# Kernel tuning notes

Measured on AMD Instinct MI355X. Metric: run time of the kernel, lower is better.

## Reference

```python
import jax, jax.numpy as jnp
import numpy as np

R = 16      # grid resolution per axis (G = R**3 voxels)
K = 8       # num KNN neighbors per voxel
H = 64      # num_hidden
NB = 2      # num conv blocks
EPS = 1e-5


def _conv3d(x, w, b):
    # x: [B,C,D,H,W], w: [O,I,3,3,3]
    y = jax.lax.conv_general_dilated(
        x, w, window_strides=(1, 1, 1), padding='SAME',
        dimension_numbers=('NCDHW', 'OIDHW', 'NCDHW'))
    return y + b[None, :, None, None, None]


def _bn(x):
    # training-mode BatchNorm3d statistics (no affine), per channel
    m = x.mean(axis=(0, 2, 3, 4), keepdims=True)
    v = x.var(axis=(0, 2, 3, 4), keepdims=True)
    return (x - m) * jax.lax.rsqrt(v + EPS)


def _forward(pos, x, pe_w1, pe_b1, pe_w2, pe_b2, f_w, f_b, up_w, up_b,
             conv_w, conv_b, on_g, on_b, ro_w, ro_b):
    B, N, _ = pos.shape
    # ---- Gridifier: coordinate grid over domain [-1, 1]^3 ----
    g1 = jnp.linspace(-1.0, 1.0, R, dtype=pos.dtype)
    grid = jnp.stack(jnp.meshgrid(g1, g1, g1, indexing='ij'), axis=-1).reshape(-1, 3)  # [G,3]
    # ---- brute-force KNN: points -> grid voxels (per graph) ----
    gn = jnp.sum(grid * grid, axis=-1)          # [G]
    pn = jnp.sum(pos * pos, axis=-1)            # [B,N]
    d = gn[None, :, None] + pn[:, None, :] - 2.0 * jnp.einsum('gc,bnc->bgn', grid, pos)  # [B,G,N]
    idx = jax.lax.top_k(jax.lax.stop_gradient(-d), K)[1]  # [B,G,K] nearest point indices
    b_ix = jnp.arange(B)[:, None, None]
    p_nb = pos[b_ix, idx]                       # [B,G,K,3] neighbor positions
    f_nb = x[b_ix, idx]                         # [B,G,K,Cin] neighbor features
    # ---- BipartiteConv: position-conditioned messages, mean aggregation ----
    rel = p_nb - grid[None, :, None, :]         # relative positions [B,G,K,3]
    pe = jax.nn.gelu(rel @ pe_w1 + pe_b1) @ pe_w2 + pe_b2   # position embed [B,G,K,H]
    msg = pe * (f_nb @ f_w + f_b)               # multiplicative conditioning [B,G,K,H]
    agg = msg.mean(axis=2)                      # [B,G,H]
    h = jax.nn.gelu(agg @ up_w + up_b)          # update net [B,G,H]
    # reshape(B,R,R,R,H).permute(0,4,3,2,1) -> NCDHW
    vol = h.reshape(B, R, R, R, H).transpose(0, 4, 3, 2, 1)  # [B,H,R,R,R]
    # ---- ConvNet3D: residual blocks, maxpool after block 0 ----
    for i in range(NB):
        h1 = jax.nn.relu(_bn(_conv3d(vol, conv_w[i, 0], conv_b[i, 0])))
        h2 = _bn(_conv3d(h1, conv_w[i, 1], conv_b[i, 1]))
        vol = jax.nn.relu(vol + h2)
        if i == 0:
            vol = jax.lax.reduce_window(vol, -jnp.inf, jax.lax.max,
                                        (1, 1, 2, 2, 2), (1, 1, 2, 2, 2), 'VALID')
    out = _bn(vol) * on_g[None, :, None, None, None] + on_b[None, :, None, None, None]
    # ---- mean readout pool + linear head ----
    pooled = out.mean(axis=(2, 3, 4))           # [B,H]
    return pooled @ ro_w + ro_b                 # [B,out_channels]


def setup_inputs() -> dict:
    key = jax.random.key(0)
    ks = jax.random.split(key, 10)
    B, N, Cin, OUT = 4, 4096, 3, 16
    s = 0.05
    return {
        'pos': jax.random.uniform(ks[0], (B, N, 3), jnp.float32, -1.0, 1.0),
        'x': jax.random.normal(ks[1], (B, N, Cin), jnp.float32),
        'pe_w1': jax.random.normal(ks[2], (3, H), jnp.float32) * 0.3,
        'pe_b1': jnp.zeros((H,), jnp.float32),
        'pe_w2': jax.random.normal(ks[3], (H, H), jnp.float32) * s,
        'pe_b2': jnp.zeros((H,), jnp.float32),
        'f_w': jax.random.normal(ks[4], (Cin, H), jnp.float32) * 0.3,
        'f_b': jnp.zeros((H,), jnp.float32),
        'up_w': jax.random.normal(ks[5], (H, H), jnp.float32) * s,
        'up_b': jnp.zeros((H,), jnp.float32),
        'conv_w': jax.random.normal(ks[6], (NB, 2, H, H, 3, 3, 3), jnp.float32) * s,
        'conv_b': jnp.zeros((NB, 2, H), jnp.float32),
        'on_g': jnp.ones((H,), jnp.float32),
        'on_b': jnp.zeros((H,), jnp.float32),
        'ro_w': jax.random.normal(ks[7], (H, OUT), jnp.float32) * s,
        'ro_b': jnp.zeros((OUT,), jnp.float32),
    }


def reference(pos, x, pe_w1, pe_b1, pe_w2, pe_b2, f_w, f_b, up_w, up_b,
              conv_w, conv_b, on_g, on_b, ro_w, ro_b):
    return _forward(pos, x, pe_w1, pe_b1, pe_w2, pe_b2, f_w, f_b, up_w, up_b,
                    conv_w, conv_b, on_g, on_b, ro_w, ro_b)
```

## Files before the change

kernel.cpp:

```cpp
#include <hip/hip_runtime.h>

#define ULL unsigned long long
typedef unsigned short ush;
typedef __attribute__((ext_vector_type(8))) short s8v;
typedef __attribute__((ext_vector_type(4))) float f4v;

#define BB 4
#define NP 4096
#define HH 64
#define EPSF 1e-5f

#define WH_OFF      0u
#define WL_OFF      221184u
#define WT_PER_CONV 110592u
#define IDX_OFF     442368u
#define VOL0_OFF    573440u
#define V0H_OFF     2066432u
#define V0L_OFF     2812928u
#define T1_OFF      3559424u
#define VOL1_OFF    4608000u
#define V1H_OFF     4864000u
#define V1L_OFF     4992000u
#define T3_OFF      5120000u
#define STATS_OFF   5251072u
#define CELLS_OFF   5251968u
#define SPOS_OFF    5268368u
#define MW_OFF      5333904u

#define ZN_V0   373248u
#define ZN_V1   64000u
#define ZN_ST   224u
#define ZN_ALL  (ZN_V0 + ZN_V1 + ZN_ST)

__device__ __forceinline__ ush f2bf(float f) {
  unsigned u = __float_as_uint(f);
  return (ush)((u + 0x7FFFu + ((u >> 16) & 1u)) >> 16);
}
__device__ __forceinline__ float bf2f(ush h) { return __uint_as_float(((unsigned)h) << 16); }

__device__ __forceinline__ float gelu_tanh(float v) {
  float inner = 0.7978845608028654f * (v + 0.044715f * v * v * v);
  return 0.5f * v * (1.0f + tanhf(inner));
}

__device__ __forceinline__ float lin16(int i) {
  return -1.0f + (float)i * (2.0f / 15.0f);
}

__global__ __launch_bounds__(256) void k_prep(const float* __restrict__ cw,
                                              const float* __restrict__ pw2,
                                              const float* __restrict__ upw,
                                              ush* __restrict__ wh,
                                              ush* __restrict__ wl,
                                              ush* __restrict__ mw,
                                              float* __restrict__ ws) {
  unsigned i = blockIdx.x * 256u + threadIdx.x;
  float4 z = make_float4(0.f, 0.f, 0.f, 0.f);
  if (i < ZN_V0) ((float4*)(ws + V0H_OFF))[i] = z;
  else if (i < ZN_V0 + ZN_V1) ((float4*)(ws + V1H_OFF))[i - ZN_V0] = z;
  else if (i < ZN_ALL) ((float4*)(ws + STATS_OFF))[i - ZN_V0 - ZN_V1] = z;
  if (i < 442368u) {
    unsigned conv = i / WT_PER_CONV;
    unsigned r = i - conv * WT_PER_CONV;
    unsigned off = r >> 12;
    unsigned q = r & 4095u;
    unsigned co = q >> 6, ci = q & 63u;
    float w = cw[(conv * 4096u + co * 64u + ci) * 27u + off];
    ush hi = f2bf(w);
    wh[i] = hi;
    wl[i] = f2bf(w - bf2f(hi));
  } else if (i < 450560u) {
    unsigned t = i - 442368u;
    unsigned mat = t >> 12, r = t & 4095u;
    unsigned co = r >> 6, ci = r & 63u;
    const float* src = mat ? upw : pw2;
    float w = src[ci * 64u + co];
    ush hi = f2bf(w);
    mw[mat * 8192u + co * 64u + ci] = hi;
    mw[mat * 8192u + 4096u + co * 64u + ci] = f2bf(w - bf2f(hi));
  }
}

__global__ __launch_bounds__(256) void k_bin(const float* __restrict__ pos,
                                             int* __restrict__ cellStart,
                                             float4* __restrict__ sortedPos) {
  __shared__ int cnt[4096];
  __shared__ int wsum[4];
  int tid = threadIdx.x;
  int b = blockIdx.x;
  const float* pb = pos + b * NP * 3;
  for (int i = tid; i < 4096; i += 256) cnt[i] = 0;
  __syncthreads();
#pragma unroll
  for (int t = 0; t < 16; ++t) {
    int p = t * 256 + tid;
    float px = pb[3 * p], py = pb[3 * p + 1], pz = pb[3 * p + 2];
    int c0 = (int)floorf((px + 1.0f) * 7.5f + 0.5f);
    int c1 = (int)floorf((py + 1.0f) * 7.5f + 0.5f);
    int c2 = (int)floorf((pz + 1.0f) * 7.5f + 0.5f);
    c0 = min(max(c0, 0), 15); c1 = min(max(c1, 0), 15); c2 = min(max(c2, 0), 15);
    atomicAdd(&cnt[(c0 * 16 + c1) * 16 + c2], 1);
  }
  __syncthreads();
  int base = tid * 16;
  int loc[16];
  int run = 0;
#pragma unroll
  for (int j = 0; j < 16; ++j) { loc[j] = run; run += cnt[base + j]; }
  int lane = tid & 63, wv = tid >> 6;
  int inc = run;
  for (int d = 1; d < 64; d <<= 1) {
    int o = __shfl_up(inc, d, 64);
    if (lane >= d) inc += o;
  }
  if (lane == 63) wsum[wv] = inc;
  __syncthreads();
  int woff = 0;
  for (int w = 0; w < wv; ++w) woff += wsum[w];
  int excl = woff + inc - run;
  __syncthreads();
  int stv[16];
#pragma unroll
  for (int j = 0; j < 16; ++j) {
    stv[j] = excl + loc[j];
    cellStart[b * 4097 + base + j] = stv[j];
  }
#pragma unroll
  for (int j = 0; j < 16; ++j) cnt[base + j] = stv[j];
  if (tid == 0) cellStart[b * 4097 + 4096] = NP;
  __syncthreads();
#pragma unroll
  for (int t = 0; t < 16; ++t) {
    int p = t * 256 + tid;
    float px = pb[3 * p], py = pb[3 * p + 1], pz = pb[3 * p + 2];
    int c0 = (int)floorf((px + 1.0f) * 7.5f + 0.5f);
    int c1 = (int)floorf((py + 1.0f) * 7.5f + 0.5f);
    int c2 = (int)floorf((pz + 1.0f) * 7.5f + 0.5f);
    c0 = min(max(c0, 0), 15); c1 = min(max(c1, 0), 15); c2 = min(max(c2, 0), 15);
    int slot = atomicAdd(&cnt[(c0 * 16 + c1) * 16 + c2], 1);
    sortedPos[b * 4096 + slot] = make_float4(px, py, pz, __int_as_float(p));
  }
}

__device__ __forceinline__ void ins8(ULL* kk, ULL key) {
  if (key < kk[7]) {
    kk[7] = key;
#pragma unroll
    for (int q = 7; q >= 1; --q) {
      ULL a = kk[q - 1], c = kk[q];
      bool sw = c < a;
      kk[q - 1] = sw ? c : a;
      kk[q] = sw ? a : c;
    }
  }
}
__device__ __forceinline__ ULL merge8(ULL* kk, int sub) {
  ULL win = 0;
#pragma unroll
  for (int r = 0; r < 8; ++r) {
    ULL m = kk[0];
#pragma unroll
    for (int s = 1; s < 8; s <<= 1) {
      ULL o = __shfl_xor(m, s, 64);
      m = (o < m) ? o : m;
    }
    if (kk[0] == m) {
#pragma unroll
      for (int q = 0; q < 7; ++q) kk[q] = kk[q + 1];
      kk[7] = ~0ULL;
    }
    if (sub == r) win = m;
  }
  return win;
}

__device__ __forceinline__ void scan_cell(const int* __restrict__ cs,
                                          const float4* __restrict__ sp,
                                          int cell, float gx, float gy, float gz,
                                          float gn, ULL* kk) {
  int st = cs[cell], en = cs[cell + 1];
  for (int p = st; p < en; ++p) {
    float4 c = sp[p];
    float pn = c.x * c.x + c.y * c.y + c.z * c.z;
    float dt = gx * c.x + gy * c.y + gz * c.z;
    float d = (gn + pn) - 2.0f * dt;
    unsigned u = __float_as_uint(d);
    u ^= (unsigned)((int)u >> 31) | 0x80000000u;
    ins8(kk, ((ULL)u << 32) | (unsigned)__float_as_uint(c.w));
  }
}

__global__ __launch_bounds__(256) void k_knn3(const int* __restrict__ cellStart,
                                              const float4* __restrict__ sortedPos,
                                              int* __restrict__ idxo) {
  int tid = threadIdx.x;
  int sub = tid & 7;
  int vox = blockIdx.x * 32 + (tid >> 3);
  int b = vox >> 12;
  int g = vox & 4095;
  int ii = g >> 8, jj = (g >> 4) & 15, kkc = g & 15;
  float gx = lin16(ii), gy = lin16(jj), gz = lin16(kkc);
  float gn = gx * gx + gy * gy + gz * gz;
  const int* cs = cellStart + b * 4097;
  const float4* sp = sortedPos + b * 4096;
  ULL kk[8];
#pragma unroll
  for (int q = 0; q < 8; ++q) kk[q] = ~0ULL;
  for (int t = sub; t < 125; t += 8) {
    int dz = t / 25, r25 = t - dz * 25;
    int a = ii + dz - 2, c1 = jj + (r25 / 5) - 2, c2 = kkc + (r25 % 5) - 2;
    if (((unsigned)a > 15u) | ((unsigned)c1 > 15u) | ((unsigned)c2 > 15u)) continue;
    scan_cell(cs, sp, (a * 16 + c1) * 16 + c2, gx, gy, gz, gn, kk);
  }
  ULL win = merge8(kk, sub);
  float bnd2 = 2.5f * (2.0f / 15.0f) - 1e-5f;
  unsigned ub2 = __float_as_uint(bnd2 * bnd2) | 0x80000000u;
  ULL w7 = __shfl(win, 7, 8);
  if (w7 >= ((ULL)ub2 << 32)) {
#pragma unroll
    for (int q = 0; q < 8; ++q) kk[q] = ~0ULL;
    for (int t = sub; t < 1331; t += 8) {
      int dz = t / 121, r = t - dz * 121;
      int a = ii + dz - 5, c1 = jj + (r / 11) - 5, c2 = kkc + (r % 11) - 5;
      if (((unsigned)a > 15u) | ((unsigned)c1 > 15u) | ((unsigned)c2 > 15u)) continue;
      scan_cell(cs, sp, (a * 16 + c1) * 16 + c2, gx, gy, gz, gn, kk);
    }
    win = merge8(kk, sub);
    float bnd5 = 5.5f * (2.0f / 15.0f) - 1e-5f;
    unsigned ub5 = __float_as_uint(bnd5 * bnd5) | 0x80000000u;
    w7 = __shfl(win, 7, 8);
    if (w7 >= ((ULL)ub5 << 32)) {
#pragma unroll
      for (int q = 0; q < 8; ++q) kk[q] = ~0ULL;
      for (int p = sub; p < NP; p += 8) {
        float4 c = sp[p];
        float pn = c.x * c.x + c.y * c.y + c.z * c.z;
        float dt = gx * c.x + gy * c.y + gz * c.z;
        float d = (gn + pn) - 2.0f * dt;
        unsigned u = __float_as_uint(d);
        u ^= (unsigned)((int)u >> 31) | 0x80000000u;
        ins8(kk, ((ULL)u << 32) | (unsigned)__float_as_uint(c.w));
      }
      win = merge8(kk, sub);
    }
  }
  idxo[(((b << 12) | g) << 3) + sub] = (int)(win & 0xFFFFFFFFULL);
}

__global__ __launch_bounds__(256) void k_mlp2(
    const float* __restrict__ pos, const float* __restrict__ xf,
    const float* __restrict__ w1, const float* __restrict__ b1,
    const float* __restrict__ b2v, const float* __restrict__ fw,
    const float* __restrict__ fb, const float* __restrict__ ub,
    const ush* __restrict__ w2tH, const ush* __restrict__ w2tL,
    const ush* __restrict__ uwtH, const ush* __restrict__ uwtL,
    const int* __restrict__ idx, float* __restrict__ vol0,
    ush* __restrict__ v0h, ush* __restrict__ v0l) {
  __shared__ __align__(16) ush lhH[128 * 72];
  __shared__ __align__(16) ush lhL[128 * 72];
  __shared__ __align__(16) float lfe[128 * 68];
  __shared__ __align__(16) ush agH[16 * 72];
  __shared__ __align__(16) ush agL[16 * 72];
  int tid = threadIdx.x, lane = tid & 63, wv = tid >> 6;
  int lm = lane & 15, quad = lane >> 4;
  int b = blockIdx.x >> 8;
  int g0 = (blockIdx.x & 255) << 4;
  s8v BH[8], BL[8], UH[2], UL[2];
#pragma unroll
  for (int n = 0; n < 4; ++n)
#pragma unroll
    for (int ks = 0; ks < 2; ++ks) {
      int o = ((n * 16 + lm) << 6) + ks * 32 + (quad << 3);
      BH[n * 2 + ks] = *(const s8v*)(w2tH + o);
      BL[n * 2 + ks] = *(const s8v*)(w2tL + o);
    }
#pragma unroll
  for (int ks = 0; ks < 2; ++ks) {
    int o = ((wv * 16 + lm) << 6) + ks * 32 + (quad << 3);
    UH[ks] = *(const s8v*)(uwtH + o);
    UL[ks] = *(const s8v*)(uwtL + o);
  }
  float w10 = w1[lane], w11 = w1[64 + lane], w12 = w1[128 + lane], b1c = b1[lane];
  float fw0 = fw[lane], fw1 = fw[64 + lane], fw2 = fw[128 + lane], fbc = fb[lane];
  float ubc = ub[wv * 16 + lm];
  float gx = lin16(g0 >> 8), gy = lin16((g0 >> 4) & 15);
  for (int i = 0; i < 32; ++i) {
    int pair = wv * 32 + i;
    int vi = pair >> 3, kk = pair & 7;
    int g = g0 + vi;
    float gz = lin16(vi);
    int p = idx[(((b << 12) | g) << 3) + kk];
    const float* pp = pos + (b * NP + p) * 3;
    float r0 = pp[0] - gx, r1 = pp[1] - gy, r2 = pp[2] - gz;
    float h1 = gelu_tanh(fmaf(r2, w12, fmaf(r1, w11, fmaf(r0, w10, b1c))));
    const float* xp = xf + (b * NP + p) * 3;
    float fe = fmaf(xp[2], fw2, fmaf(xp[1], fw1, fmaf(xp[0], fw0, fbc)));
    ush hi = f2bf(h1);
    lhH[pair * 72 + lane] = hi;
    lhL[pair * 72 + lane] = f2bf(h1 - bf2f(hi));
    lfe[pair * 68 + lane] = fe;
  }
  f4v acc[2][4];
#pragma unroll
  for (int m = 0; m < 2; ++m)
#pragma unroll
    for (int n = 0; n < 4; ++n) acc[m][n] = (f4v){0.f, 0.f, 0.f, 0.f};
#pragma unroll
  for (int m = 0; m < 2; ++m)
#pragma unroll
    for (int ks = 0; ks < 2; ++ks) {
      int ao = (wv * 32 + m * 16 + lm) * 72 + ks * 32 + quad * 8;
      s8v Ah = *(const s8v*)&lhH[ao];
      s8v Al = *(const s8v*)&lhL[ao];
#pragma unroll
      for (int n = 0; n < 4; ++n) {
        acc[m][n] = __builtin_amdgcn_mfma_f32_16x16x32_bf16(Ah, BH[n * 2 + ks], acc[m][n], 0, 0, 0);
        acc[m][n] = __builtin_amdgcn_mfma_f32_16x16x32_bf16(Ah, BL[n * 2 + ks], acc[m][n], 0, 0, 0);
        acc[m][n] = __builtin_amdgcn_mfma_f32_16x16x32_bf16(Al, BH[n * 2 + ks], acc[m][n], 0, 0, 0);
      }
    }
  float b2c[4];
#pragma unroll
  for (int n = 0; n < 4; ++n) b2c[n] = b2v[n * 16 + lm];
#pragma unroll
  for (int m = 0; m < 2; ++m) {
    int vox = wv * 4 + m * 2 + (quad >> 1);
#pragma unroll
    for (int n = 0; n < 4; ++n) {
      float s = 0.0f;
#pragma unroll
      for (int r = 0; r < 4; ++r) {
        int pair = wv * 32 + m * 16 + quad * 4 + r;
        s += (acc[m][n][r] + b2c[n]) * lfe[pair * 68 + n * 16 + lm];
      }
      s += __shfl_xor(s, 16, 64);
      s *= 0.125f;
      if ((quad & 1) == 0) {
        ush hi = f2bf(s);
        agH[vox * 72 + n * 16 + lm] = hi;
        agL[vox * 72 + n * 16 + lm] = f2bf(s - bf2f(hi));
      }
    }
  }
  __syncthreads();
  f4v a2 = (f4v){0.f, 0.f, 0.f, 0.f};
#pragma unroll
  for (int ks = 0; ks < 2; ++ks) {
    int ao = lm * 72 + ks * 32 + quad * 8;
    s8v Ah = *(const s8v*)&agH[ao];
    s8v Al = *(const s8v*)&agL[ao];
    a2 = __builtin_amdgcn_mfma_f32_16x16x32_bf16(Ah, UH[ks], a2, 0, 0, 0);
    a2 = __builtin_amdgcn_mfma_f32_16x16x32_bf16(Ah, UL[ks], a2, 0, 0, 0);
    a2 = __builtin_amdgcn_mfma_f32_16x16x32_bf16(Al, UH[ks], a2, 0, 0, 0);
  }
  int xc = g0 >> 8, yc = (g0 >> 4) & 15;
#pragma unroll
  for (int r = 0; r < 4; ++r) {
    int vox = quad * 4 + r;
    float h = gelu_tanh(a2[r] + ubc);
    int pidx = (((b * 18 + vox + 1) * 18 + yc + 1) * 18 + xc + 1) * 64 + wv * 16 + lm;
    vol0[pidx] = h;
    ush hi = f2bf(h);
    v0h[pidx] = hi;
    v0l[pidx] = f2bf(h - bf2f(hi));
  }
}

template <int Z>
__global__ __launch_bounds__(256) void k_convm(const ush* __restrict__ vh,
                                               const ush* __restrict__ vl,
                                               const ush* __restrict__ wh,
                                               const ush* __restrict__ wl,
                                               float* __restrict__ out,
                                               float* __restrict__ stats) {
  constexpr int P = Z + 2;
  constexpr int Py = (Z == 16) ? 6 : 10;
  constexpr int Px = (Z == 16) ? 18 : 10;
  constexpr int NV = 3 * Py * Px;
  constexpr int VS = 272;
  __shared__ unsigned char slab[NV * VS];
  __shared__ float ls[64], ls2[64];
  int tid = threadIdx.x;
  int lane = tid & 63, wv = tid >> 6;
  int vbase = blockIdx.x * 64;
  int b = (Z == 16) ? (vbase >> 12) : (vbase >> 9);
  int rem = vbase & (Z * Z * Z - 1);
  int z0 = rem / (Z * Z);
  int y0 = (Z == 16) ? ((rem & 255) >> 4) : 0;
  if (tid < 64) { ls[tid] = 0.0f; ls2[tid] = 0.0f; }
  {
    constexpr int NCH = NV * 8;
    for (int i = tid; i < NCH; i += 256) {
      int v = i >> 3, c = i & 7;
      int lz = v / (Py * Px);
      int r = v - lz * (Py * Px);
      int ly = r / Px, lx = r - ly * Px;
      int g = (((b * P + z0 + lz) * P + (y0 + ly)) * P + lx) * 64 + c * 8;
      *(uint4*)(slab + v * VS + c * 16)       = *(const uint4*)(vh + g);
      *(uint4*)(slab + v * VS + 128 + c * 16) = *(const uint4*)(vl + g);
    }
  }
  __syncthreads();
  int lm = lane & 15, quad = lane >> 4;
  int co = (wv << 4) | lm;
  f4v acc[4];
#pragma unroll
  for (int m = 0; m < 4; ++m) acc[m] = (f4v){0.f, 0.f, 0.f, 0.f};
  for (int off = 0; off < 27; ++off) {
    int dz = off / 9, r9 = off - dz * 9, dy = r9 / 3, dx = r9 - dy * 3;
    const ush* bph = wh + ((off * 64 + co) << 6) + (quad << 3);
    const ush* bpl = wl + ((off * 64 + co) << 6) + (quad << 3);
#pragma unroll
    for (int ks = 0; ks < 2; ++ks) {
      s8v bhf = *(const s8v*)(bph + ks * 32);
      s8v blf = *(const s8v*)(bpl + ks * 32);
#pragma unroll
      for (int m = 0; m < 4; ++m) {
        int lyp, lxp;
        if (Z == 16) { lyp = m + dy; lxp = lm + dx; }
        else         { lyp = 2 * m + (lm >> 3) + dy; lxp = (lm & 7) + dx; }
        int sv = (dz * Py + lyp) * Px + lxp;
        const unsigned char* ap = slab + sv * VS + (quad << 4) + (ks << 6);
        s8v ahf = *(const s8v*)(ap);
        s8v alf = *(const s8v*)(ap + 128);
        acc[m] = __builtin_amdgcn_mfma_f32_16x16x32_bf16(ahf, bhf, acc[m], 0, 0, 0);
        acc[m] = __builtin_amdgcn_mfma_f32_16x16x32_bf16(ahf, blf, acc[m], 0, 0, 0);
        acc[m] = __builtin_amdgcn_mfma_f32_16x16x32_bf16(alf, bhf, acc[m], 0, 0, 0);
      }
    }
  }
  float s = 0.0f, s2 = 0.0f;
#pragma unroll
  for (int m = 0; m < 4; ++m) {
    int vx = vbase + (m << 4) + (quad << 2);
#pragma unroll
    for (int r = 0; r < 4; ++r) {
      float v = acc[m][r];
      out[(vx + r) * 64 + co] = v;
      s += v;
      s2 = fmaf(v, v, s2);
    }
  }
  atomicAdd(&ls[co], s);
  atomicAdd(&ls2[co], s2);
  __syncthreads();
  if (tid < 64) {
    atomicAdd(&stats[tid * 2], ls[tid]);
    atomicAdd(&stats[tid * 2 + 1], ls2[tid]);
  }
}

template <int Z>
__global__ __launch_bounds__(256) void k_bnrelu(const float* __restrict__ t,
                                                const float* __restrict__ stats,
                                                ush* __restrict__ outh,
                                                ush* __restrict__ outl,
                                                float inv_cnt) {
  constexpr int P = Z + 2;
  unsigned i = blockIdx.x * 256u + threadIdx.x;
  int c = i & 63;
  int vox = i >> 6;
  int x = vox % Z;
  int q = vox / Z;
  int y = q % Z;
  q /= Z;
  int z = q % Z;
  int b = q / Z;
  float m = stats[c * 2] * inv_cnt;
  float var = stats[c * 2 + 1] * inv_cnt - m * m;
  float rs = 1.0f / sqrtf(var + EPSF);
  float v = (t[i] - m) * rs;
  v = v > 0.0f ? v : 0.0f;
  int pidx = (((b * P + z + 1) * P + y + 1) * P + x + 1) * 64 + c;
  ush hi = f2bf(v);
  outh[pidx] = hi;
  outl[pidx] = f2bf(v - bf2f(hi));
}

__global__ __launch_bounds__(256) void k_residpool(const float* __restrict__ vol0,
                                                   const float* __restrict__ t2,
                                                   const float* __restrict__ stats,
                                                   float* __restrict__ vol1,
                                                   ush* __restrict__ v1h,
                                                   ush* __restrict__ v1l) {
  unsigned i = blockIdx.x * 256u + threadIdx.x;
  int c = i & 63;
  int pv = i >> 6;
  int xp = pv & 7, yp = (pv >> 3) & 7, zp = (pv >> 6) & 7, b = pv >> 9;
  float m = stats[c * 2] * (1.0f / 16384.0f);
  float var = stats[c * 2 + 1] * (1.0f / 16384.0f) - m * m;
  float rs = 1.0f / sqrtf(var + EPSF);
  float best = 0.0f;
  for (int dz = 0; dz < 2; ++dz)
    for (int dy = 0; dy < 2; ++dy)
      for (int dx = 0; dx < 2; ++dx) {
        int z = 2 * zp + dz, y = 2 * yp + dy, x = 2 * xp + dx;
        float a = vol0[(((b * 18 + z + 1) * 18 + y + 1) * 18 + x + 1) * 64 + c];
        float t = t2[(b * 4096 + z * 256 + y * 16 + x) * 64 + c];
        float u = a + (t - m) * rs;
        u = u > 0.0f ? u : 0.0f;
        best = u > best ? u : best;
      }
  int pidx = (((b * 10 + zp + 1) * 10 + yp + 1) * 10 + xp + 1) * 64 + c;
  vol1[pidx] = best;
  ush hi = f2bf(best);
  v1h[pidx] = hi;
  v1l[pidx] = f2bf(best - bf2f(hi));
}

__global__ __launch_bounds__(256) void k_resid2(const float* __restrict__ vol1,
                                                const float* __restrict__ t4,
                                                const float* __restrict__ stats,
                                                float* __restrict__ sF,
                                                float* __restrict__ sB) {
  __shared__ float ls[64], ls2[64];
  if (threadIdx.x < 64) { ls[threadIdx.x] = 0.0f; ls2[threadIdx.x] = 0.0f; }
  __syncthreads();
  unsigned i = blockIdx.x * 256u + threadIdx.x;
  int c = i & 63;
  int pv = i >> 6;
  int x = pv & 7, y = (pv >> 3) & 7, z = (pv >> 6) & 7, b = pv >> 9;
  float m = stats[c * 2] * (1.0f / 2048.0f);
  float var = stats[c * 2 + 1] * (1.0f / 2048.0f) - m * m;
  float rs = 1.0f / sqrtf(var + EPSF);
  float a = vol1[(((b * 10 + z + 1) * 10 + y + 1) * 10 + x + 1) * 64 + c];
  float u = a + (t4[i] - m) * rs;
  u = u > 0.0f ? u : 0.0f;
  atomicAdd(&ls[c], u);
  atomicAdd(&ls2[c], u * u);
  __syncthreads();
  if (threadIdx.x < 64) {
    int cc = threadIdx.x;
    atomicAdd(&sF[cc * 2], ls[cc]);
    atomicAdd(&sF[cc * 2 + 1], ls2[cc]);
    atomicAdd(&sB[b * 64 + cc], ls[cc]);
  }
}

__global__ __launch_bounds__(64) void k_final(const float* __restrict__ sF,
                                              const float* __restrict__ sB,
                                              const float* __restrict__ ong,
                                              const float* __restrict__ onb,
                                              const float* __restrict__ row,
                                              const float* __restrict__ rob,
                                              float* __restrict__ outp) {
  __shared__ float pl[4][64];
  int c = threadIdx.x;
  float m = sF[c * 2] * (1.0f / 2048.0f);
  float var = sF[c * 2 + 1] * (1.0f / 2048.0f) - m * m;
  float rs = 1.0f / sqrtf(var + EPSF);
  float gg = ong[c], bb = onb[c];
  for (int b = 0; b < 4; ++b)
    pl[b][c] = (sB[b * 64 + c] * (1.0f / 512.0f) - m) * rs * gg + bb;
  __syncthreads();
  int b = threadIdx.x >> 4, o = threadIdx.x & 15;
  float s = rob[o];
  for (int j = 0; j < 64; ++j) s = fmaf(pl[b][j], row[j * 16 + o], s);
  outp[b * 16 + o] = s;
}

extern "C" void kernel_launch(void* const* d_in, const int* in_sizes, int n_in,
                              void* d_out, int out_size, void* d_ws, size_t ws_size,
                              hipStream_t stream) {
  (void)in_sizes; (void)n_in; (void)out_size; (void)ws_size;
  const float* pos = (const float*)d_in[0];
  const float* xf  = (const float*)d_in[1];
  const float* pw1 = (const float*)d_in[2];
  const float* pb1 = (const float*)d_in[3];
  const float* pw2 = (const float*)d_in[4];
  const float* pb2 = (const float*)d_in[5];
  const float* fw  = (const float*)d_in[6];
  const float* fb  = (const float*)d_in[7];
  const float* uw  = (const float*)d_in[8];
  const float* ubp = (const float*)d_in[9];
  const float* cw  = (const float*)d_in[10];
  const float* ong = (const float*)d_in[12];
  const float* onb = (const float*)d_in[13];
  const float* row = (const float*)d_in[14];
  const float* rob = (const float*)d_in[15];

  float* ws   = (float*)d_ws;
  ush*   wh   = (ush*)(ws + WH_OFF);
  ush*   wl   = (ush*)(ws + WL_OFF);
  int*   idx  = (int*)(ws + IDX_OFF);
  float* vol0 = ws + VOL0_OFF;
  ush*   v0h  = (ush*)(ws + V0H_OFF);
  ush*   v0l  = (ush*)(ws + V0L_OFF);
  float* t1   = ws + T1_OFF;
  float* vol1 = ws + VOL1_OFF;
  ush*   v1h  = (ush*)(ws + V1H_OFF);
  ush*   v1l  = (ush*)(ws + V1L_OFF);
  float* t3   = ws + T3_OFF;
  float* sA   = ws + STATS_OFF;
  float* sF   = sA + 512;
  float* sB   = sF + 128;
  int*   cellStart = (int*)(ws + CELLS_OFF);
  float4* sortedPos = (float4*)(ws + SPOS_OFF);
  ush*   mw   = (ush*)(ws + MW_OFF);

  k_prep<<<1760, 256, 0, stream>>>(cw, pw2, uw, wh, wl, mw, ws);
  k_bin<<<4, 256, 0, stream>>>(pos, cellStart, sortedPos);
  k_knn3<<<512, 256, 0, stream>>>(cellStart, sortedPos, idx);
  k_mlp2<<<1024, 256, 0, stream>>>(pos, xf, pw1, pb1, pb2, fw, fb, ubp,
                                   mw, mw + 4096, mw + 8192, mw + 12288,
                                   idx, vol0, v0h, v0l);
  k_convm<16><<<256, 256, 0, stream>>>(v0h, v0l, wh, wl, t1, sA);
  k_bnrelu<16><<<4096, 256, 0, stream>>>(t1, sA, v0h, v0l, 1.0f / 16384.0f);
  k_convm<16><<<256, 256, 0, stream>>>(v0h, v0l, wh + WT_PER_CONV, wl + WT_PER_CONV,
                                       t1, sA + 128);
  k_residpool<<<512, 256, 0, stream>>>(vol0, t1, sA + 128, vol1, v1h, v1l);
  k_convm<8><<<32, 256, 0, stream>>>(v1h, v1l, wh + 2 * WT_PER_CONV,
                                     wl + 2 * WT_PER_CONV, t3, sA + 256);
  k_bnrelu<8><<<512, 256, 0, stream>>>(t3, sA + 256, v1h, v1l, 1.0f / 2048.0f);
  k_convm<8><<<32, 256, 0, stream>>>(v1h, v1l, wh + 3 * WT_PER_CONV,
                                     wl + 3 * WT_PER_CONV, t3, sA + 384);
  k_resid2<<<512, 256, 0, stream>>>(vol1, t3, sA + 384, sF, sB);
  k_final<<<1, 64, 0, stream>>>(sF, sB, ong, onb, row, rob, (float*)d_out);
}
```

Measured before the change: 367.2 us.

## Tile KNN over 4x4x4 voxel blocks with shared candidate buffer

KNN now assigns each block a 4x4x4 voxel tile. The block stages every point from the surrounding cell region in shared memory, and each voxel is scanned by 4 lanes instead of 8. The fallback bound is computed from the staged region's distance to its edges. The weight prep kernel now reads conv weights coalesced and scatters the writes, and the MLP kernel gathers neighbor pos/features once into shared memory. These changes aim to cut redundant global loads, at the cost of more per-thread insertion work and some shared-memory pressure.

```diff
diff --git a/kernel.cpp b/kernel.cpp
--- a/kernel.cpp
+++ b/kernel.cpp
@@ -62,13 +62,15 @@
   if (i < 442368u) {
     unsigned conv = i / WT_PER_CONV;
     unsigned r = i - conv * WT_PER_CONV;
-    unsigned off = r >> 12;
-    unsigned q = r & 4095u;
-    unsigned co = q >> 6, ci = q & 63u;
-    float w = cw[(conv * 4096u + co * 64u + ci) * 27u + off];
+    unsigned co = r / 1728u;
+    unsigned r2 = r - co * 1728u;
+    unsigned ci = r2 / 27u;
+    unsigned off = r2 - ci * 27u;
+    float w = cw[i];
     ush hi = f2bf(w);
-    wh[i] = hi;
-    wl[i] = f2bf(w - bf2f(hi));
+    unsigned dst = conv * WT_PER_CONV + (off * 64u + co) * 64u + ci;
+    wh[dst] = hi;
+    wl[dst] = f2bf(w - bf2f(hi));
   } else if (i < 450560u) {
     unsigned t = i - 442368u;
     unsigned mat = t >> 12, r = t & 4095u;
@@ -154,24 +156,19 @@
     }
   }
 }
-__device__ __forceinline__ ULL merge8(ULL* kk, int sub) {
-  ULL win = 0;
+__device__ __forceinline__ void merge4(ULL* kk, int sub, ULL& win0, ULL& win1) {
 #pragma unroll
   for (int r = 0; r < 8; ++r) {
     ULL m = kk[0];
-#pragma unroll
-    for (int s = 1; s < 8; s <<= 1) {
-      ULL o = __shfl_xor(m, s, 64);
-      m = (o < m) ? o : m;
-    }
+    ULL o = __shfl_xor(m, 1, 64); m = (o < m) ? o : m;
+    o = __shfl_xor(m, 2, 64);     m = (o < m) ? o : m;
     if (kk[0] == m) {
 #pragma unroll
       for (int q = 0; q < 7; ++q) kk[q] = kk[q + 1];
       kk[7] = ~0ULL;
     }
-    if (sub == r) win = m;
-  }
-  return win;
+    if (sub == (r & 3)) { if (r < 4) win0 = m; else win1 = m; }
+  }
 }
 
 __device__ __forceinline__ void scan_cell(const int* __restrict__ cs,
@@ -190,49 +187,109 @@
   }
 }
 
-__global__ __launch_bounds__(256) void k_knn3(const int* __restrict__ cellStart,
+__global__ __launch_bounds__(256) void k_knn4(const int* __restrict__ cellStart,
                                               const float4* __restrict__ sortedPos,
                                               int* __restrict__ idxo) {
+  constexpr int CAP = 3072;
+  __shared__ float4 pts[CAP];
+  __shared__ int rst[128], rlen[128], rof[128];
+  __shared__ int Tsh;
   int tid = threadIdx.x;
-  int sub = tid & 7;
-  int vox = blockIdx.x * 32 + (tid >> 3);
-  int b = vox >> 12;
-  int g = vox & 4095;
-  int ii = g >> 8, jj = (g >> 4) & 15, kkc = g & 15;
+  int lane = tid & 63;
+  int sub = tid & 3;
+  int lv = tid >> 2;
+  int tile = blockIdx.x;
+  int b = tile >> 6;
+  int t6 = tile & 63;
+  int ii0 = (t6 >> 4) * 4, jj0 = ((t6 >> 2) & 3) * 4, kk0 = (t6 & 3) * 4;
+  int ii = ii0 + (lv >> 4), jj = jj0 + ((lv >> 2) & 3), kkc = kk0 + (lv & 3);
+  int g = (ii << 8) | (jj << 4) | kkc;
   float gx = lin16(ii), gy = lin16(jj), gz = lin16(kkc);
   float gn = gx * gx + gy * gy + gz * gz;
   const int* cs = cellStart + b * 4097;
   const float4* sp = sortedPos + b * 4096;
+  int loa = max(ii0 - 3, 0), hia = min(ii0 + 6, 15);
+  int lob = max(jj0 - 3, 0), hib = min(jj0 + 6, 15);
+  int loc = max(kk0 - 3, 0), hic = min(kk0 + 6, 15);
+  int Ra = hia - loa + 1, Rb = hib - lob + 1;
+  int nrows = Ra * Rb;
+  if (tid < 128) {
+    int st = 0, len = 0;
+    if (tid < nrows) {
+      int a = loa + tid / Rb, c1 = lob + tid % Rb;
+      int base = (a * 16 + c1) * 16;
+      st = cs[base + loc];
+      len = cs[base + hic + 1] - st;
+    }
+    rst[tid] = st;
+    rlen[tid] = len;
+  }
+  __syncthreads();
+  if (tid < 64) {
+    int l0v = rlen[lane], l1v = rlen[lane + 64];
+    int s0 = l0v;
+    for (int d = 1; d < 64; d <<= 1) { int o = __shfl_up(s0, d, 64); if (lane >= d) s0 += o; }
+    int tot0 = __shfl(s0, 63, 64);
+    int s1 = l1v;
+    for (int d = 1; d < 64; d <<= 1) { int o = __shfl_up(s1, d, 64); if (lane >= d) s1 += o; }
+    int tot1 = __shfl(s1, 63, 64);
+    rof[lane] = s0 - l0v;
+    rof[lane + 64] = tot0 + s1 - l1v;
+    if (lane == 0) Tsh = tot0 + tot1;
+  }
+  __syncthreads();
+  int T = Tsh;
+  if (T <= CAP) {
+    for (int i = tid; i < T; i += 256) {
+      int lo = 0, hi = nrows - 1;
+      while (lo < hi) { int mid = (lo + hi + 1) >> 1; if (rof[mid] <= i) lo = mid; else hi = mid - 1; }
+      pts[i] = sp[rst[lo] + (i - rof[lo])];
+    }
+  }
+  __syncthreads();
   ULL kk[8];
 #pragma unroll
   for (int q = 0; q < 8; ++q) kk[q] = ~0ULL;
-  for (int t = sub; t < 125; t += 8) {
-    int dz = t / 25, r25 = t - dz * 25;
-    int a = ii + dz - 2, c1 = jj + (r25 / 5) - 2, c2 = kkc + (r25 % 5) - 2;
-    if (((unsigned)a > 15u) | ((unsigned)c1 > 15u) | ((unsigned)c2 > 15u)) continue;
-    scan_cell(cs, sp, (a * 16 + c1) * 16 + c2, gx, gy, gz, gn, kk);
-  }
-  ULL win = merge8(kk, sub);
-  float bnd2 = 2.5f * (2.0f / 15.0f) - 1e-5f;
-  unsigned ub2 = __float_as_uint(bnd2 * bnd2) | 0x80000000u;
-  ULL w7 = __shfl(win, 7, 8);
-  if (w7 >= ((ULL)ub2 << 32)) {
+  if (T <= CAP) {
+    for (int i = sub; i < T; i += 4) {
+      float4 c = pts[i];
+      float pn = c.x * c.x + c.y * c.y + c.z * c.z;
+      float dt = gx * c.x + gy * c.y + gz * c.z;
+      float d = (gn + pn) - 2.0f * dt;
+      unsigned u = __float_as_uint(d);
+      u ^= (unsigned)((int)u >> 31) | 0x80000000u;
+      ins8(kk, ((ULL)u << 32) | (unsigned)__float_as_uint(c.w));
+    }
+  }
+  ULL win0 = ~0ULL, win1 = ~0ULL;
+  merge4(kk, sub, win0, win1);
+  ULL w7 = __shfl(win1, lane | 3, 64);
+  int dmin = 100;
+  if (loa > 0)  dmin = min(dmin, ii - loa + 1);
+  if (hia < 15) dmin = min(dmin, hia + 1 - ii);
+  if (lob > 0)  dmin = min(dmin, jj - lob + 1);
+  if (hib < 15) dmin = min(dmin, hib + 1 - jj);
+  if (loc > 0)  dmin = min(dmin, kkc - loc + 1);
+  if (hic < 15) dmin = min(dmin, hic + 1 - kkc);
+  float bnd = ((float)dmin - 0.5f) * (2.0f / 15.0f) - 1e-5f;
+  ULL ubk = ((ULL)(__float_as_uint(bnd * bnd) | 0x80000000u)) << 32;
+  if (w7 >= ubk) {
 #pragma unroll
     for (int q = 0; q < 8; ++q) kk[q] = ~0ULL;
-    for (int t = sub; t < 1331; t += 8) {
+    for (int t = sub; t < 1331; t += 4) {
       int dz = t / 121, r = t - dz * 121;
       int a = ii + dz - 5, c1 = jj + (r / 11) - 5, c2 = kkc + (r % 11) - 5;
       if (((unsigned)a > 15u) | ((unsigned)c1 > 15u) | ((unsigned)c2 > 15u)) continue;
       scan_cell(cs, sp, (a * 16 + c1) * 16 + c2, gx, gy, gz, gn, kk);
     }
-    win = merge8(kk, sub);
+    merge4(kk, sub, win0, win1);
     float bnd5 = 5.5f * (2.0f / 15.0f) - 1e-5f;
-    unsigned ub5 = __float_as_uint(bnd5 * bnd5) | 0x80000000u;
-    w7 = __shfl(win, 7, 8);
-    if (w7 >= ((ULL)ub5 << 32)) {
+    ULL ub5 = ((ULL)(__float_as_uint(bnd5 * bnd5) | 0x80000000u)) << 32;
+    w7 = __shfl(win1, lane | 3, 64);
+    if (w7 >= ub5) {
 #pragma unroll
       for (int q = 0; q < 8; ++q) kk[q] = ~0ULL;
-      for (int p = sub; p < NP; p += 8) {
+      for (int p = sub; p < NP; p += 4) {
         float4 c = sp[p];
         float pn = c.x * c.x + c.y * c.y + c.z * c.z;
         float dt = gx * c.x + gy * c.y + gz * c.z;
@@ -241,10 +298,12 @@
         u ^= (unsigned)((int)u >> 31) | 0x80000000u;
         ins8(kk, ((ULL)u << 32) | (unsigned)__float_as_uint(c.w));
       }
-      win = merge8(kk, sub);
-    }
-  }
-  idxo[(((b << 12) | g) << 3) + sub] = (int)(win & 0xFFFFFFFFULL);
+      merge4(kk, sub, win0, win1);
+    }
+  }
+  int addr = (((b << 12) | g) << 3);
+  idxo[addr + sub] = (int)(win0 & 0xFFFFFFFFULL);
+  idxo[addr + sub + 4] = (int)(win1 & 0xFFFFFFFFULL);
 }
 
 __global__ __launch_bounds__(256) void k_mlp2(
@@ -261,6 +320,7 @@
   __shared__ __align__(16) float lfe[128 * 68];
   __shared__ __align__(16) ush agH[16 * 72];
   __shared__ __align__(16) ush agL[16 * 72];
+  __shared__ float gpb[128 * 8];
   int tid = threadIdx.x, lane = tid & 63, wv = tid >> 6;
   int lm = lane & 15, quad = lane >> 4;
   int b = blockIdx.x >> 8;
@@ -280,21 +340,28 @@
     UH[ks] = *(const s8v*)(uwtH + o);
     UL[ks] = *(const s8v*)(uwtL + o);
   }
+  if (tid < 128) {
+    int vi = tid >> 3, kp = tid & 7;
+    int g = g0 + vi;
+    int p = idx[(((b << 12) | g) << 3) + kp];
+    const float* pp = pos + (b * NP + p) * 3;
+    const float* xp = xf + (b * NP + p) * 3;
+    gpb[tid * 8 + 0] = pp[0]; gpb[tid * 8 + 1] = pp[1]; gpb[tid * 8 + 2] = pp[2];
+    gpb[tid * 8 + 3] = xp[0]; gpb[tid * 8 + 4] = xp[1]; gpb[tid * 8 + 5] = xp[2];
+  }
   float w10 = w1[lane], w11 = w1[64 + lane], w12 = w1[128 + lane], b1c = b1[lane];
   float fw0 = fw[lane], fw1 = fw[64 + lane], fw2 = fw[128 + lane], fbc = fb[lane];
   float ubc = ub[wv * 16 + lm];
   float gx = lin16(g0 >> 8), gy = lin16((g0 >> 4) & 15);
+  __syncthreads();
   for (int i = 0; i < 32; ++i) {
     int pair = wv * 32 + i;
-    int vi = pair >> 3, kk = pair & 7;
-    int g = g0 + vi;
+    int vi = pair >> 3;
     float gz = lin16(vi);
-    int p = idx[(((b << 12) | g) << 3) + kk];
-    const float* pp = pos + (b * NP + p) * 3;
-    float r0 = pp[0] - gx, r1 = pp[1] - gy, r2 = pp[2] - gz;
+    float r0 = gpb[pair * 8 + 0] - gx, r1 = gpb[pair * 8 + 1] - gy, r2 = gpb[pair * 8 + 2] - gz;
     float h1 = gelu_tanh(fmaf(r2, w12, fmaf(r1, w11, fmaf(r0, w10, b1c))));
-    const float* xp = xf + (b * NP + p) * 3;
-    float fe = fmaf(xp[2], fw2, fmaf(xp[1], fw1, fmaf(xp[0], fw0, fbc)));
+    float fe = fmaf(gpb[pair * 8 + 5], fw2,
+                    fmaf(gpb[pair * 8 + 4], fw1, fmaf(gpb[pair * 8 + 3], fw0, fbc)));
     ush hi = f2bf(h1);
     lhH[pair * 72 + lane] = hi;
     lhL[pair * 72 + lane] = f2bf(h1 - bf2f(hi));
@@ -600,7 +667,7 @@
 
   k_prep<<<1760, 256, 0, stream>>>(cw, pw2, uw, wh, wl, mw, ws);
   k_bin<<<4, 256, 0, stream>>>(pos, cellStart, sortedPos);
-  k_knn3<<<512, 256, 0, stream>>>(cellStart, sortedPos, idx);
+  k_knn4<<<256, 256, 0, stream>>>(cellStart, sortedPos, idx);
   k_mlp2<<<1024, 256, 0, stream>>>(pos, xf, pw1, pb1, pb2, fw, fb, ubp,
                                    mw, mw + 4096, mw + 8192, mw + 12288,
                                    idx, vol0, v0h, v0l);
```

Result: faster. 345.7 us (-5.9%).
